# Kernel tuning notes

Hardware: AMD Instinct MI355X
Metric: run time of the kernel (lower is better)

The kernel has to match this reference:

```python
import jax, jax.numpy as jnp
import numpy as np

EMBED_DIM = 1024
HEAD_NUM = 16
HEAD_DIM = EMBED_DIM // HEAD_NUM
T, B, S = 2048, 4, 2048


def setup_inputs() -> dict:
    key = jax.random.key(0)
    ks = jax.random.split(key, 11)
    s = 0.02
    return {
        "query": jax.random.normal(ks[0], (T, B, EMBED_DIM), jnp.float32),
        "key": jax.random.normal(ks[1], (S, B, EMBED_DIM), jnp.float32),
        "value": jax.random.normal(ks[2], (S, B, EMBED_DIM), jnp.float32),
        "q_proj_weight": jax.random.normal(ks[3], (EMBED_DIM, EMBED_DIM), jnp.float32) * s,
        "k_proj_weight": jax.random.normal(ks[4], (EMBED_DIM, EMBED_DIM), jnp.float32) * s,
        "v_proj_weight": jax.random.normal(ks[5], (EMBED_DIM, EMBED_DIM), jnp.float32) * s,
        "in_proj_bias": jax.random.normal(ks[6], (3 * EMBED_DIM,), jnp.float32) * s,
        "bias_k": jax.random.normal(ks[7], (1, 1, EMBED_DIM), jnp.float32) * s,
        "bias_v": jax.random.normal(ks[8], (1, 1, EMBED_DIM), jnp.float32) * s,
        "out_proj_weight": jax.random.normal(ks[9], (EMBED_DIM, EMBED_DIM), jnp.float32) * s,
        "out_proj_bias": jax.random.normal(ks[10], (EMBED_DIM,), jnp.float32) * s,
    }


def reference(query, key, value, q_proj_weight, k_proj_weight, v_proj_weight,
              in_proj_bias, bias_k, bias_v, out_proj_weight, out_proj_bias):
    t, b, e = query.shape
    h, hd = HEAD_NUM, HEAD_DIM
    scaling = float(hd) ** -0.5
    # input projections (F.linear: x @ W.T + b)
    q = (query @ q_proj_weight.T + in_proj_bias[:e]) * scaling          # [T,B,E]
    k = key @ k_proj_weight.T + in_proj_bias[e:2 * e]                   # [S,B,E]
    v = value @ v_proj_weight.T + in_proj_bias[2 * e:]                  # [S,B,E]
    # append bias_k / bias_v token along the sequence dim
    k = jnp.concatenate([k, jnp.broadcast_to(bias_k, (1, b, e))], axis=0)  # [S+1,B,E]
    v = jnp.concatenate([v, jnp.broadcast_to(bias_v, (1, b, e))], axis=0)  # [S+1,B,E]
    # split heads: [L, B, E] -> [B*H, L, hd]
    q = q.reshape(t, b * h, hd).transpose(1, 0, 2)
    k = k.reshape(-1, b * h, hd).transpose(1, 0, 2)
    v = v.reshape(-1, b * h, hd).transpose(1, 0, 2)
    # full O(T*S) attention, as in the original bmm->softmax->bmm
    weights = jax.nn.softmax(jnp.einsum('nqd,nkd->nqk', q, k), axis=-1)  # [B*H,T,S+1]
    out = jnp.einsum('nqk,nkd->nqd', weights, v)                         # [B*H,T,hd]
    out = out.transpose(1, 0, 2).reshape(t, b, e)
    out = out @ out_proj_weight.T + out_proj_bias
    avg_weights = weights.sum(axis=1) / h                                # [B*H,S+1]
    return out, avg_weights
```

## Files before the change

### kernel.cpp

```cpp
#include <hip/hip_runtime.h>

#define T_DIM 2048
#define B_DIM 4
#define S_DIM 2048
#define E_DIM 1024
#define H_NUM 16
#define HD    64
#define NH    64
#define SP1   2049
#define SPAD  2112
#define NCHUNK 33

typedef short bf16x8 __attribute__((ext_vector_type(8)));
typedef float f32x4  __attribute__((ext_vector_type(4)));
typedef float f32x16 __attribute__((ext_vector_type(16)));
typedef unsigned int u32;

#define QSCALE 0.18033688011112042f

#if __has_builtin(__builtin_amdgcn_exp2f)
__device__ __forceinline__ float exp2_fast(float x) { return __builtin_amdgcn_exp2f(x); }
#else
__device__ __forceinline__ float exp2_fast(float x) { return __expf(x * 0.6931471805599453f); }
#endif

__device__ __forceinline__ unsigned short f2bf(float x) {
    union { float f; unsigned int u; } v; v.f = x;
    unsigned int r = v.u + 0x7FFFu + ((v.u >> 16) & 1u);
    return (unsigned short)(r >> 16);
}

__device__ __forceinline__ u32 cvtpk_bf16(float lo, float hi) {
    u32 r;
    asm("v_cvt_pk_bf16_f32 %0, %1, %2" : "=v"(r) : "v"(lo), "v"(hi));
    return r;
}
__device__ __forceinline__ void plswap(u32& a, u32& b) {
    asm("v_permlane32_swap_b32 %0, %1" : "+v"(a), "+v"(b));
}

__global__ __launch_bounds__(256)
void cvt_bf16_k(const float* __restrict__ src, short* __restrict__ dst, int n8)
{
    int i = blockIdx.x * 256 + threadIdx.x;
    if (i >= n8) return;
    const float4* s = reinterpret_cast<const float4*>(src) + (size_t)i * 2;
    float4 a = s[0], b = s[1];
    bf16x8 o;
    o[0] = (short)f2bf(a.x); o[1] = (short)f2bf(a.y);
    o[2] = (short)f2bf(a.z); o[3] = (short)f2bf(a.w);
    o[4] = (short)f2bf(b.x); o[5] = (short)f2bf(b.y);
    o[6] = (short)f2bf(b.z); o[7] = (short)f2bf(b.w);
    *(reinterpret_cast<bf16x8*>(dst) + i) = o;
}

template<int MODE>
__global__ __launch_bounds__(256)
void gemm_bf16(const void* __restrict__ Ap, const short* __restrict__ W,
               const float* __restrict__ bias, void* __restrict__ outp)
{
    __shared__ short As[128][72];
    __shared__ short Bs[128][72];
    const int bm = blockIdx.x, bn = blockIdx.y;
    const int tid = threadIdx.x;
    const int l = tid & 63, w = tid >> 6;
    const int wr = w >> 1, wc = w & 1;
    const int lr = l & 15, lg = l >> 4;

    f32x4 acc[4][4] = {};

    for (int k0 = 0; k0 < E_DIM; k0 += 64) {
#pragma unroll
        for (int it = 0; it < 4; ++it) {
            const int idx = it * 256 + tid;
            const int row = idx >> 3, cg = idx & 7;
            if (MODE == 3) {
                const int m = bm * 128 + row;
                const size_t asrc =
                    ((size_t)((m & 3) * 16 + (k0 >> 6)) * T_DIM + (m >> 2)) * HD + cg * 8;
                *reinterpret_cast<bf16x8*>(&As[row][cg * 8]) =
                    *reinterpret_cast<const bf16x8*>((const short*)Ap + asrc);
            } else {
                const float* ap = (const float*)Ap + (size_t)(bm * 128 + row) * E_DIM + k0 + cg * 8;
                const float4 a0 = *reinterpret_cast<const float4*>(ap);
                const float4 a1 = *reinterpret_cast<const float4*>(ap + 4);
                uint4 st;
                st.x = cvtpk_bf16(a0.x, a0.y); st.y = cvtpk_bf16(a0.z, a0.w);
                st.z = cvtpk_bf16(a1.x, a1.y); st.w = cvtpk_bf16(a1.z, a1.w);
                *reinterpret_cast<uint4*>(&As[row][cg * 8]) = st;
            }
            *reinterpret_cast<bf16x8*>(&Bs[row][cg * 8]) =
                *reinterpret_cast<const bf16x8*>(W + (size_t)(bn * 128 + row) * E_DIM + k0 + cg * 8);
        }
        __syncthreads();
        __builtin_amdgcn_s_setprio(1);
#pragma unroll
        for (int c = 0; c < 2; ++c) {
            bf16x8 af[4], bf[4];
#pragma unroll
            for (int mi = 0; mi < 4; ++mi)
                af[mi] = *reinterpret_cast<const bf16x8*>(&As[wr * 64 + mi * 16 + lr][c * 32 + lg * 8]);
#pragma unroll
            for (int ni = 0; ni < 4; ++ni)
                bf[ni] = *reinterpret_cast<const bf16x8*>(&Bs[wc * 64 + ni * 16 + lr][c * 32 + lg * 8]);
#pragma unroll
            for (int mi = 0; mi < 4; ++mi)
#pragma unroll
                for (int ni = 0; ni < 4; ++ni)
                    acc[mi][ni] = __builtin_amdgcn_mfma_f32_16x16x32_bf16(
                        af[mi], bf[ni], acc[mi][ni], 0, 0, 0);
        }
        __builtin_amdgcn_s_setprio(0);
        __syncthreads();
    }

#pragma unroll
    for (int mi = 0; mi < 4; ++mi)
#pragma unroll
        for (int ni = 0; ni < 4; ++ni) {
            const int colg = bn * 128 + wc * 64 + ni * 16 + lr;
            const float bv = bias[colg];
#pragma unroll
            for (int r = 0; r < 4; ++r) {
                const int m = bm * 128 + wr * 64 + mi * 16 + lg * 4 + r;
                float v = acc[mi][ni][r] + bv;
                if (MODE == 3) {
                    ((float*)outp)[(size_t)m * E_DIM + colg] = v;
                } else {
                    if (MODE == 0) v *= QSCALE;
                    const int seq = m >> 2, b = m & 3;
                    const int head = colg >> 6, d = colg & 63;
                    const int sd = (MODE == 0) ? T_DIM : SPAD;
                    ((short*)outp)[((size_t)(b * 16 + head) * sd + seq) * HD + d] = (short)f2bf(v);
                }
            }
        }
}

__global__ void fill_kv_pad(short* __restrict__ k_h, short* __restrict__ v_h,
                            const float* __restrict__ bias_k,
                            const float* __restrict__ bias_v)
{
    const int d   = threadIdx.x;
    const int row = S_DIM + blockIdx.x;
    const int n   = blockIdx.y;
    short bk = 0, bv = 0;
    if (row == S_DIM) {
        bk = (short)f2bf(bias_k[(n & 15) * HD + d]);
        bv = (short)f2bf(bias_v[(n & 15) * HD + d]);
    }
    const size_t idx = ((size_t)n * SPAD + row) * HD + d;
    k_h[idx] = bk;
    v_h[idx] = bv;
}

__global__ __launch_bounds__(256)
void attn_mfma(const short* __restrict__ q_h, const short* __restrict__ k_h,
               const short* __restrict__ v_h, short* __restrict__ o_h,
               float* __restrict__ m_arr, float* __restrict__ l_arr)
{
    __shared__ short KsD[2][64 * 64];
    __shared__ short VtD[2][64 * 64];

    const int n = blockIdx.y, q0 = blockIdx.x * 128;
    const int tid = threadIdx.x, l = tid & 63, w = tid >> 6;
    const int ql = l & 31;
    const int hi = l >> 5;
    const int qrow = q0 + w * 32 + ql;

    const int krow = tid >> 3, kcg = tid & 7;
    const int kswz = (kcg * 16) ^ ((krow & 7) << 4);
    const int sp = tid & 31, d0 = (tid >> 5) * 8;

    const short* kbase = k_h + (size_t)n * SPAD * HD;
    const short* vbase = v_h + (size_t)n * SPAD * HD;

    bf16x8 aq0, aq1, aq2, aq3;
    {
        const short* qp = q_h + ((size_t)n * T_DIM + qrow) * HD + hi * 8;
        aq0 = *(const bf16x8*)(qp);
        aq1 = *(const bf16x8*)(qp + 16);
        aq2 = *(const bf16x8*)(qp + 32);
        aq3 = *(const bf16x8*)(qp + 48);
    }

    bf16x8 pk0 = *(const bf16x8*)(kbase + (size_t)krow * HD + kcg * 8);
    bf16x8 pk1 = *(const bf16x8*)(kbase + (size_t)(32 + krow) * HD + kcg * 8);
    bf16x8 pv0 = *(const bf16x8*)(vbase + (size_t)(2 * sp) * HD + d0);
    bf16x8 pv1 = *(const bf16x8*)(vbase + (size_t)(2 * sp + 1) * HD + d0);
    {
        char* KsB = (char*)KsD[0];
        char* VtB = (char*)VtD[0];
        *(bf16x8*)(KsB + krow * 128 + kswz) = pk0;
        *(bf16x8*)(KsB + (32 + krow) * 128 + kswz) = pk1;
#pragma unroll
        for (int j = 0; j < 8; ++j) {
            u32 pk = (u32)(unsigned short)pv0[j] | ((u32)(unsigned short)pv1[j] << 16);
            const int d = d0 + j;
            *(u32*)(VtB + d * 128 + ((4 * sp) ^ ((d & 7) << 4))) = pk;
        }
    }
    __syncthreads();

    float m_run = -1e30f, l_run = 0.f;
    f32x16 accA, accB;
#pragma unroll
    for (int r = 0; r < 16; ++r) { accA[r] = 0.f; accB[r] = 0.f; }

    for (int kc = 0; kc < NCHUNK; ++kc) {
        const char* KsB = (const char*)KsD[kc & 1];
        const char* VtB = (const char*)VtD[kc & 1];
        const bool more = (kc + 1 < NCHUNK);

        if (more) {
            const int s0n = (kc + 1) * 64;
            pk0 = *(const bf16x8*)(kbase + (size_t)(s0n + krow) * HD + kcg * 8);
            pk1 = *(const bf16x8*)(kbase + (size_t)(s0n + 32 + krow) * HD + kcg * 8);
            pv0 = *(const bf16x8*)(vbase + (size_t)(s0n + 2 * sp) * HD + d0);
            pv1 = *(const bf16x8*)(vbase + (size_t)(s0n + 2 * sp + 1) * HD + d0);
        }

        f32x16 sc0, sc1;
#pragma unroll
        for (int r = 0; r < 16; ++r) { sc0[r] = 0.f; sc1[r] = 0.f; }
        __builtin_amdgcn_s_setprio(1);
#pragma unroll
        for (int sl = 0; sl < 4; ++sl) {
            const int cb = ((sl * 32) + hi * 16) ^ ((ql & 7) << 4);
            bf16x8 kf0 = *(const bf16x8*)(KsB + ql * 128 + cb);
            bf16x8 kf1 = *(const bf16x8*)(KsB + (32 + ql) * 128 + cb);
            bf16x8 qf = (sl == 0) ? aq0 : (sl == 1) ? aq1 : (sl == 2) ? aq2 : aq3;
            sc0 = __builtin_amdgcn_mfma_f32_32x32x16_bf16(kf0, qf, sc0, 0, 0, 0);
            sc1 = __builtin_amdgcn_mfma_f32_32x32x16_bf16(kf1, qf, sc1, 0, 0, 0);
        }
        __builtin_amdgcn_s_setprio(0);

        const int s0 = kc * 64;
        if (s0 + 64 > SP1) {
#pragma unroll
            for (int r = 0; r < 16; ++r) {
                const int key = (r & 3) + 8 * (r >> 2) + 4 * hi;
                if (s0 + key >= SP1)      sc0[r] = -1e30f;
                if (s0 + 32 + key >= SP1) sc1[r] = -1e30f;
            }
        }

        float mx = sc0[0];
#pragma unroll
        for (int r = 1; r < 16; ++r) mx = fmaxf(mx, sc0[r]);
#pragma unroll
        for (int r = 0; r < 16; ++r) mx = fmaxf(mx, sc1[r]);
        mx = fmaxf(mx, __shfl_xor(mx, 32));
        if (!__all(mx - m_run <= 8.0f)) {
            const float mnew = fmaxf(m_run, mx);
            const float fac = exp2_fast(m_run - mnew);
            l_run *= fac;
#pragma unroll
            for (int r = 0; r < 16; ++r) { accA[r] *= fac; accB[r] *= fac; }
            m_run = mnew;
        }
        float ps = 0.f;
        float p0[16], p1[16];
#pragma unroll
        for (int r = 0; r < 16; ++r) { p0[r] = exp2_fast(sc0[r] - m_run); ps += p0[r]; }
#pragma unroll
        for (int r = 0; r < 16; ++r) { p1[r] = exp2_fast(sc1[r] - m_run); ps += p1[r]; }
        ps += __shfl_xor(ps, 32);
        l_run += ps;

        union PF { u32 u[4]; bf16x8 v; };
        PF pf0, pf1, pf2, pf3;
        {
            u32 a0 = cvtpk_bf16(p0[0], p0[1]),   b0 = cvtpk_bf16(p0[4], p0[5]);   plswap(a0, b0);
            u32 a1 = cvtpk_bf16(p0[2], p0[3]),   b1 = cvtpk_bf16(p0[6], p0[7]);   plswap(a1, b1);
            u32 a2 = cvtpk_bf16(p0[8], p0[9]),   b2 = cvtpk_bf16(p0[12], p0[13]); plswap(a2, b2);
            u32 a3 = cvtpk_bf16(p0[10], p0[11]), b3 = cvtpk_bf16(p0[14], p0[15]); plswap(a3, b3);
            pf0.u[0] = a0; pf0.u[1] = a1; pf0.u[2] = b0; pf0.u[3] = b1;
            pf1.u[0] = a2; pf1.u[1] = a3; pf1.u[2] = b2; pf1.u[3] = b3;
            u32 c0 = cvtpk_bf16(p1[0], p1[1]),   d0_ = cvtpk_bf16(p1[4], p1[5]);   plswap(c0, d0_);
            u32 c1 = cvtpk_bf16(p1[2], p1[3]),   d1_ = cvtpk_bf16(p1[6], p1[7]);   plswap(c1, d1_);
            u32 c2 = cvtpk_bf16(p1[8], p1[9]),   d2_ = cvtpk_bf16(p1[12], p1[13]); plswap(c2, d2_);
            u32 c3 = cvtpk_bf16(p1[10], p1[11]), d3_ = cvtpk_bf16(p1[14], p1[15]); plswap(c3, d3_);
            pf2.u[0] = c0; pf2.u[1] = c1; pf2.u[2] = d0_; pf2.u[3] = d1_;
            pf3.u[0] = c2; pf3.u[1] = c3; pf3.u[2] = d2_; pf3.u[3] = d3_;
        }

        __builtin_amdgcn_s_setprio(1);
#pragma unroll
        for (int ksl = 0; ksl < 4; ++ksl) {
            const int cb = ((ksl * 32) + hi * 16) ^ ((ql & 7) << 4);
            bf16x8 vf0 = *(const bf16x8*)(VtB + ql * 128 + cb);
            bf16x8 vf1 = *(const bf16x8*)(VtB + (32 + ql) * 128 + cb);
            const bf16x8 pv = (ksl == 0) ? pf0.v : (ksl == 1) ? pf1.v : (ksl == 2) ? pf2.v : pf3.v;
            accA = __builtin_amdgcn_mfma_f32_32x32x16_bf16(vf0, pv, accA, 0, 0, 0);
            accB = __builtin_amdgcn_mfma_f32_32x32x16_bf16(vf1, pv, accB, 0, 0, 0);
        }
        __builtin_amdgcn_s_setprio(0);

        if (more) {
            char* KsN = (char*)KsD[(kc & 1) ^ 1];
            char* VtN = (char*)VtD[(kc & 1) ^ 1];
            *(bf16x8*)(KsN + krow * 128 + kswz) = pk0;
            *(bf16x8*)(KsN + (32 + krow) * 128 + kswz) = pk1;
#pragma unroll
            for (int j = 0; j < 8; ++j) {
                u32 pk = (u32)(unsigned short)pv0[j] | ((u32)(unsigned short)pv1[j] << 16);
                const int d = d0 + j;
                *(u32*)(VtN + d * 128 + ((4 * sp) ^ ((d & 7) << 4))) = pk;
            }
            __syncthreads();
        }
    }

    const float il = 1.0f / l_run;
    short* orow = o_h + ((size_t)n * T_DIM + qrow) * HD;
#pragma unroll
    for (int rq = 0; rq < 4; ++rq) {
        uint2 st;
        st.x = cvtpk_bf16(accA[rq * 4 + 0] * il, accA[rq * 4 + 1] * il);
        st.y = cvtpk_bf16(accA[rq * 4 + 2] * il, accA[rq * 4 + 3] * il);
        *(uint2*)(orow + rq * 8 + hi * 4) = st;
        uint2 st2;
        st2.x = cvtpk_bf16(accB[rq * 4 + 0] * il, accB[rq * 4 + 1] * il);
        st2.y = cvtpk_bf16(accB[rq * 4 + 2] * il, accB[rq * 4 + 3] * il);
        *(uint2*)(orow + 32 + rq * 8 + hi * 4) = st2;
    }
    if (hi == 0) {
        m_arr[n * T_DIM + qrow] = m_run;
        l_arr[n * T_DIM + qrow] = l_run;
    }
}

__global__ __launch_bounds__(256)
void colsum_mfma(const short* __restrict__ q_h, const short* __restrict__ k_h,
                 const float* __restrict__ m_arr, const float* __restrict__ l_arr,
                 float* __restrict__ avg_out)
{
    __shared__ short Qs[2][64][72];
    __shared__ float msh[2][64];
    __shared__ float lih[2][64];

    const int n = blockIdx.y, s0 = blockIdx.x * 64;
    const int tid = threadIdx.x, l = tid & 63, w = tid >> 6;
    const int lr = l & 15, lg = l >> 4;
    const int qr = tid >> 3, qcg = tid & 7;

    const short* qbase = q_h + (size_t)n * T_DIM * HD;

    bf16x8 ak[2];
#pragma unroll
    for (int c = 0; c < 2; ++c)
        ak[c] = *reinterpret_cast<const bf16x8*>(
            k_h + ((size_t)n * SPAD + s0 + w * 16 + lr) * HD + c * 32 + lg * 8);

    bf16x8 qa = *(const bf16x8*)(qbase + (size_t)qr * HD + qcg * 8);
    bf16x8 qb = *(const bf16x8*)(qbase + (size_t)(32 + qr) * HD + qcg * 8);
    float mlv = 0.f;
    if (tid < 64) mlv = m_arr[n * T_DIM + tid];
    else if (tid < 128) mlv = l_arr[n * T_DIM + tid - 64];
    *(bf16x8*)&Qs[0][qr][qcg * 8] = qa;
    *(bf16x8*)&Qs[0][32 + qr][qcg * 8] = qb;
    if (tid < 64) msh[0][tid] = mlv;
    else if (tid < 128) lih[0][tid - 64] = 1.0f / mlv;
    __syncthreads();

    float csum[4] = {0.f, 0.f, 0.f, 0.f};

    for (int it = 0; it < T_DIM / 64; ++it) {
        const int buf = it & 1;
        const bool more = (it + 1 < T_DIM / 64);
        if (more) {
            const int qo = (it + 1) * 64;
            qa = *(const bf16x8*)(qbase + (size_t)(qo + qr) * HD + qcg * 8);
            qb = *(const bf16x8*)(qbase + (size_t)(qo + 32 + qr) * HD + qcg * 8);
            if (tid < 64) mlv = m_arr[n * T_DIM + qo + tid];
            else if (tid < 128) mlv = l_arr[n * T_DIM + qo + tid - 64];
        }
        __builtin_amdgcn_s_setprio(1);
#pragma unroll
        for (int qt = 0; qt < 4; ++qt) {
            bf16x8 bq0 = *reinterpret_cast<const bf16x8*>(&Qs[buf][qt * 16 + lr][lg * 8]);
            bf16x8 bq1 = *reinterpret_cast<const bf16x8*>(&Qs[buf][qt * 16 + lr][32 + lg * 8]);
            f32x4 z = {0.f, 0.f, 0.f, 0.f};
            z = __builtin_amdgcn_mfma_f32_16x16x32_bf16(ak[0], bq0, z, 0, 0, 0);
            z = __builtin_amdgcn_mfma_f32_16x16x32_bf16(ak[1], bq1, z, 0, 0, 0);
            const float mq = msh[buf][qt * 16 + lr];
            const float lq = lih[buf][qt * 16 + lr];
#pragma unroll
            for (int r = 0; r < 4; ++r)
                csum[r] += exp2_fast(z[r] - mq) * lq;
        }
        __builtin_amdgcn_s_setprio(0);
        if (more) {
            *(bf16x8*)&Qs[buf ^ 1][qr][qcg * 8] = qa;
            *(bf16x8*)&Qs[buf ^ 1][32 + qr][qcg * 8] = qb;
            if (tid < 64) msh[buf ^ 1][tid] = mlv;
            else if (tid < 128) lih[buf ^ 1][tid - 64] = 1.0f / mlv;
            __syncthreads();
        }
    }

#pragma unroll
    for (int r = 0; r < 4; ++r) {
        float v = csum[r];
        v += __shfl_xor(v, 1, 16);
        v += __shfl_xor(v, 2, 16);
        v += __shfl_xor(v, 4, 16);
        v += __shfl_xor(v, 8, 16);
        if (lr == 0) {
            const int key = s0 + w * 16 + lg * 4 + r;
            if (key < SP1) avg_out[(size_t)n * SP1 + key] = v * 0.0625f;
        }
    }
}

extern "C" void kernel_launch(void* const* d_in, const int* in_sizes, int n_in,
                              void* d_out, int out_size, void* d_ws, size_t ws_size,
                              hipStream_t stream)
{
    const float* query   = (const float*)d_in[0];
    const float* key     = (const float*)d_in[1];
    const float* value   = (const float*)d_in[2];
    const float* wq      = (const float*)d_in[3];
    const float* wk      = (const float*)d_in[4];
    const float* wv      = (const float*)d_in[5];
    const float* in_bias = (const float*)d_in[6];
    const float* bias_k  = (const float*)d_in[7];
    const float* bias_v  = (const float*)d_in[8];
    const float* wo      = (const float*)d_in[9];
    const float* out_b   = (const float*)d_in[10];
    float* out = (float*)d_out;

    short* wqb = (short*)d_ws;
    short* wkb = wqb + (size_t)E_DIM * E_DIM;
    short* wvb = wkb + (size_t)E_DIM * E_DIM;
    short* wob = wvb + (size_t)E_DIM * E_DIM;
    short* q_h = wob + (size_t)E_DIM * E_DIM;
    short* k_h = q_h + (size_t)NH * T_DIM * HD;
    short* v_h = k_h + (size_t)NH * SPAD * HD;
    short* o_h = v_h + (size_t)NH * SPAD * HD;
    float* m_arr = (float*)(o_h + (size_t)NH * T_DIM * HD);
    float* l_arr = m_arr + (size_t)NH * T_DIM;

    const int n8_w = E_DIM * E_DIM / 8;
    const dim3 blk(256);
    hipLaunchKernelGGL(cvt_bf16_k, dim3((n8_w + 255) / 256), blk, 0, stream, wq, wqb, n8_w);
    hipLaunchKernelGGL(cvt_bf16_k, dim3((n8_w + 255) / 256), blk, 0, stream, wk, wkb, n8_w);
    hipLaunchKernelGGL(cvt_bf16_k, dim3((n8_w + 255) / 256), blk, 0, stream, wv, wvb, n8_w);
    hipLaunchKernelGGL(cvt_bf16_k, dim3((n8_w + 255) / 256), blk, 0, stream, wo, wob, n8_w);

    const dim3 gg(64, 8);
    hipLaunchKernelGGL((gemm_bf16<0>), gg, blk, 0, stream, (const void*)query, wqb, in_bias,             (void*)q_h);
    hipLaunchKernelGGL((gemm_bf16<1>), gg, blk, 0, stream, (const void*)key,   wkb, in_bias + E_DIM,     (void*)k_h);
    hipLaunchKernelGGL((gemm_bf16<2>), gg, blk, 0, stream, (const void*)value, wvb, in_bias + 2 * E_DIM, (void*)v_h);
    hipLaunchKernelGGL(fill_kv_pad, dim3(SPAD - S_DIM, NH), dim3(64), 0, stream,
                       k_h, v_h, bias_k, bias_v);
    hipLaunchKernelGGL(attn_mfma, dim3(T_DIM / 128, NH), blk, 0, stream,
                       q_h, k_h, v_h, o_h, m_arr, l_arr);
    hipLaunchKernelGGL(colsum_mfma, dim3(NCHUNK, NH), blk, 0, stream,
                       q_h, k_h, m_arr, l_arr, out + (size_t)T_DIM * B_DIM * E_DIM);
    hipLaunchKernelGGL((gemm_bf16<3>), gg, blk, 0, stream, (const void*)o_h, wob, out_b, (void*)out);
}
```

Measured before the change: 303.5 us.

## Register-prefetch GEMM tiles and remap attention blocks so each head stays on one XCD

The GEMM kernel now loads the next K-tile from global memory into registers while MFMAs run on the current shared-memory tile, then writes it to LDS between two barriers. This hides global-load latency at the cost of extra registers and an added barrier per iteration. The attention and colsum kernels switch to a 1D grid whose block IDs are remapped so that all blocks of a given head land on the same XCD, which should improve L2 reuse of K/V.

```diff
diff --git a/kernel.cpp b/kernel.cpp
--- a/kernel.cpp
+++ b/kernel.cpp
@@ -66,33 +66,56 @@
     const int l = tid & 63, w = tid >> 6;
     const int wr = w >> 1, wc = w & 1;
     const int lr = l & 15, lg = l >> 4;
-
-    f32x4 acc[4][4] = {};
-
-    for (int k0 = 0; k0 < E_DIM; k0 += 64) {
+    const int rb = tid >> 3, cg = tid & 7;
+
+    float4 paA[4], paB[4];
+    bf16x8 pa3[4];
+    bf16x8 pb[4];
+
+    auto load_tiles = [&](int k0) {
 #pragma unroll
         for (int it = 0; it < 4; ++it) {
-            const int idx = it * 256 + tid;
-            const int row = idx >> 3, cg = idx & 7;
+            const int row = it * 32 + rb;
             if (MODE == 3) {
                 const int m = bm * 128 + row;
                 const size_t asrc =
                     ((size_t)((m & 3) * 16 + (k0 >> 6)) * T_DIM + (m >> 2)) * HD + cg * 8;
-                *reinterpret_cast<bf16x8*>(&As[row][cg * 8]) =
-                    *reinterpret_cast<const bf16x8*>((const short*)Ap + asrc);
+                pa3[it] = *reinterpret_cast<const bf16x8*>((const short*)Ap + asrc);
             } else {
                 const float* ap = (const float*)Ap + (size_t)(bm * 128 + row) * E_DIM + k0 + cg * 8;
-                const float4 a0 = *reinterpret_cast<const float4*>(ap);
-                const float4 a1 = *reinterpret_cast<const float4*>(ap + 4);
+                paA[it] = *reinterpret_cast<const float4*>(ap);
+                paB[it] = *reinterpret_cast<const float4*>(ap + 4);
+            }
+            pb[it] = *reinterpret_cast<const bf16x8*>(
+                W + (size_t)(bn * 128 + row) * E_DIM + k0 + cg * 8);
+        }
+    };
+    auto write_tiles = [&]() {
+#pragma unroll
+        for (int it = 0; it < 4; ++it) {
+            const int row = it * 32 + rb;
+            if (MODE == 3) {
+                *reinterpret_cast<bf16x8*>(&As[row][cg * 8]) = pa3[it];
+            } else {
                 uint4 st;
-                st.x = cvtpk_bf16(a0.x, a0.y); st.y = cvtpk_bf16(a0.z, a0.w);
-                st.z = cvtpk_bf16(a1.x, a1.y); st.w = cvtpk_bf16(a1.z, a1.w);
+                st.x = cvtpk_bf16(paA[it].x, paA[it].y); st.y = cvtpk_bf16(paA[it].z, paA[it].w);
+                st.z = cvtpk_bf16(paB[it].x, paB[it].y); st.w = cvtpk_bf16(paB[it].z, paB[it].w);
                 *reinterpret_cast<uint4*>(&As[row][cg * 8]) = st;
             }
-            *reinterpret_cast<bf16x8*>(&Bs[row][cg * 8]) =
-                *reinterpret_cast<const bf16x8*>(W + (size_t)(bn * 128 + row) * E_DIM + k0 + cg * 8);
-        }
-        __syncthreads();
+            *reinterpret_cast<bf16x8*>(&Bs[row][cg * 8]) = pb[it];
+        }
+    };
+
+    load_tiles(0);
+    write_tiles();
+    __syncthreads();
+
+    f32x4 acc[4][4] = {};
+
+    for (int k0 = 0; k0 < E_DIM; k0 += 64) {
+        const bool more = (k0 + 64 < E_DIM);
+        if (more) load_tiles(k0 + 64);
+
         __builtin_amdgcn_s_setprio(1);
 #pragma unroll
         for (int c = 0; c < 2; ++c) {
@@ -111,7 +134,12 @@
                         af[mi], bf[ni], acc[mi][ni], 0, 0, 0);
         }
         __builtin_amdgcn_s_setprio(0);
-        __syncthreads();
+
+        if (more) {
+            __syncthreads();
+            write_tiles();
+            __syncthreads();
+        }
     }
 
 #pragma unroll
@@ -162,7 +190,11 @@
     __shared__ short KsD[2][64 * 64];
     __shared__ short VtD[2][64 * 64];
 
-    const int n = blockIdx.y, q0 = blockIdx.x * 128;
+    const int id = blockIdx.x;
+    const int xcd = id & 7, slot = id >> 3;
+    const int n = xcd * 8 + (slot >> 4);
+    const int q0 = (slot & 15) * 128;
+
     const int tid = threadIdx.x, l = tid & 63, w = tid >> 6;
     const int ql = l & 31;
     const int hi = l >> 5;
@@ -340,7 +372,11 @@
     __shared__ float msh[2][64];
     __shared__ float lih[2][64];
 
-    const int n = blockIdx.y, s0 = blockIdx.x * 64;
+    const int id = blockIdx.x;
+    const int xcd = id & 7, slot = id >> 3;
+    const int n = xcd * 8 + slot / 33;
+    const int s0 = (slot % 33) * 64;
+
     const int tid = threadIdx.x, l = tid & 63, w = tid >> 6;
     const int lr = l & 15, lg = l >> 4;
     const int qr = tid >> 3, qcg = tid & 7;
@@ -455,9 +491,9 @@
     hipLaunchKernelGGL((gemm_bf16<2>), gg, blk, 0, stream, (const void*)value, wvb, in_bias + 2 * E_DIM, (void*)v_h);
     hipLaunchKernelGGL(fill_kv_pad, dim3(SPAD - S_DIM, NH), dim3(64), 0, stream,
                        k_h, v_h, bias_k, bias_v);
-    hipLaunchKernelGGL(attn_mfma, dim3(T_DIM / 128, NH), blk, 0, stream,
+    hipLaunchKernelGGL(attn_mfma, dim3(1024), blk, 0, stream,
                        q_h, k_h, v_h, o_h, m_arr, l_arr);
-    hipLaunchKernelGGL(colsum_mfma, dim3(NCHUNK, NH), blk, 0, stream,
+    hipLaunchKernelGGL(colsum_mfma, dim3(2112), blk, 0, stream,
                        q_h, k_h, m_arr, l_arr, out + (size_t)T_DIM * B_DIM * E_DIM);
     hipLaunchKernelGGL((gemm_bf16<3>), gg, blk, 0, stream, (const void*)o_h, wob, out_b, (void*)out);
 }
```

Measured after the change: 309.6 us. 2.0% more time.
